# Kernel optimization log

Measured on AMD Instinct MI355X. Metric: run time of the kernel, lower is better.

Reference implementation:

```python
import jax, jax.numpy as jnp
import numpy as np

B, S, D_MODEL, HEADS, DK = 2, 2048, 1024, 16, 64


def setup_inputs() -> dict:
    key = jax.random.key(0)
    ks = jax.random.split(key, 7)
    scale = 0.02
    return {
        "query": jax.random.normal(ks[0], (B, S, D_MODEL), jnp.float32),
        "key": jax.random.normal(ks[1], (B, S, D_MODEL), jnp.float32),
        "value": jax.random.normal(ks[2], (B, S, D_MODEL), jnp.float32),
        "Wq": jax.random.normal(ks[3], (D_MODEL, HEADS * DK), jnp.float32) * scale,
        "bq": jax.random.normal(ks[4], (HEADS * DK,), jnp.float32) * scale,
        "Wo": jax.random.normal(ks[5], (HEADS * DK, D_MODEL), jnp.float32) * scale,
        "bo": jax.random.normal(ks[6], (D_MODEL,), jnp.float32) * scale,
    }


def reference(query, key, value, Wq, bq, Wo, bo):
    # NOTE: faithful to the original code, which (buggily) uses _W_q to
    # project query, key AND value, and scales by sqrt(seq_len), not sqrt(d_k).
    seq_len = key.shape[1]

    def split_heads(x):
        # [B,S,H*DK] -> [H,B,S,DK]; torch chunk(dim=-1)+cat(dim=0) stacks head h
        # (slice h*DK:(h+1)*DK) at batch block h.
        p = x @ Wq + bq
        b, s, _ = p.shape
        return p.reshape(b, s, HEADS, DK).transpose(2, 0, 1, 3)

    q = split_heads(query)   # [H,B,S,DK]
    k = split_heads(key)
    v = split_heads(value)

    inv_scale = jnp.float32(1.0 / np.sqrt(seq_len))
    scores = jnp.einsum("hbqd,hbkd->hbqk", q, k) * inv_scale  # [H,B,S,S]
    attn = jax.nn.softmax(scores, axis=-1)
    out = jnp.einsum("hbqk,hbkd->hbqd", attn, v)  # [H,B,S,DK]
    # inverse of chunk(dim=0)+cat(dim=-1): [H,B,S,DK] -> [B,S,H*DK]
    out = out.transpose(1, 2, 0, 3).reshape(query.shape[0], query.shape[1], HEADS * DK)
    return out @ Wo + bo
```

## Files before the change

### kernel.cpp

```cpp
#include <hip/hip_runtime.h>

#define DEVI __device__ __forceinline__

typedef short short4_t __attribute__((ext_vector_type(4)));
typedef short short8_t __attribute__((ext_vector_type(8)));
typedef __bf16 bf16x8 __attribute__((ext_vector_type(8)));
typedef float f32x4 __attribute__((ext_vector_type(4)));

DEVI short f2bf(float f) {
    union { float f; unsigned u; } v; v.f = f;
    unsigned r = (v.u + 0x7fffu + ((v.u >> 16) & 1u)) >> 16;
    return (short)r;
}

DEVI unsigned pack_ru(float a, float b) {
    union { float f; unsigned u; } x, y; x.f = a; y.f = b;
    return __builtin_amdgcn_perm(y.u + 0x8000u, x.u + 0x8000u, 0x07060302u);
}

DEVI f32x4 pv_mfma(short4_t a, short4_t b, f32x4 c) {
#if defined(__HIP_DEVICE_COMPILE__)
#if __has_builtin(__builtin_amdgcn_mfma_f32_16x16x16bf16_1k)
    return __builtin_amdgcn_mfma_f32_16x16x16bf16_1k(a, b, c, 0, 0, 0);
#else
    union { short8_t s; bf16x8 b; } ua, ub;
    ua.s = (short8_t){a[0], a[1], a[2], a[3], 0, 0, 0, 0};
    ub.s = (short8_t){b[0], b[1], b[2], b[3], 0, 0, 0, 0};
    return __builtin_amdgcn_mfma_f32_16x16x32_bf16(ua.b, ub.b, c, 0, 0, 0);
#endif
#else
    (void)a; (void)b;
    return c;
#endif
}

DEVI void g2lds16(const short* g, short* l) {
    __builtin_amdgcn_global_load_lds(
        (const __attribute__((address_space(1))) void*)g,
        (__attribute__((address_space(3))) void*)l, 16, 0, 0);
}

__global__ __launch_bounds__(256) void cvt3_kernel(const float* __restrict__ q,
                                                   const float* __restrict__ k,
                                                   const float* __restrict__ v,
                                                   short* __restrict__ X) {
    const size_t N1 = (size_t)4096 * 1024;
    size_t e = ((size_t)blockIdx.x * 256 + threadIdx.x) * 4;
    const float* src; size_t off;
    if (e < N1)            { src = q; off = e; }
    else if (e < 2 * N1)   { src = k; off = e - N1; }
    else                   { src = v; off = e - 2 * N1; }
    f32x4 f = *(const f32x4*)(src + off);
    short4_t o;
    o[0] = f2bf(f[0]); o[1] = f2bf(f[1]); o[2] = f2bf(f[2]); o[3] = f2bf(f[3]);
    *(short4_t*)(X + e) = o;
}

__global__ __launch_bounds__(256) void transpose_w_kernel(const float* __restrict__ W,
                                                          short* __restrict__ Wt) {
    __shared__ short T[64][65];
    const int t = threadIdx.x;
    const int kt = blockIdx.x * 64, nt = blockIdx.y * 64;
#pragma unroll
    for (int r = 0; r < 4; ++r) {
        int kl = (t >> 4) + 16 * r;
        int n0 = (t & 15) * 4;
        f32x4 f = *(const f32x4*)(W + (size_t)(kt + kl) * 1024 + nt + n0);
#pragma unroll
        for (int j = 0; j < 4; ++j) T[n0 + j][kl] = f2bf(f[j]);
    }
    __syncthreads();
#pragma unroll
    for (int r = 0; r < 2; ++r) {
        int nl = (t >> 3) + 32 * r;
        int k0 = (t & 7) * 8;
        short8_t v;
#pragma unroll
        for (int j = 0; j < 8; ++j) v[j] = T[nl][k0 + j];
        *(short8_t*)(Wt + (size_t)(nt + nl) * 1024 + kt + k0) = v;
    }
}

template <typename OutT>
__global__ __launch_bounds__(256) void gemm_bt_kernel(const short* __restrict__ A,
                                                      const short* __restrict__ Bt,
                                                      const float* __restrict__ bias,
                                                      OutT* __restrict__ C,
                                                      int M, int N, int K,
                                                      int qrows, float qscale) {
    __shared__ __align__(16) short As[128 * 32];
    __shared__ __align__(16) short Bs[128 * 32];
    const int tid  = threadIdx.x;
    const int lane = tid & 63, wave = tid >> 6;
    const int quad = lane >> 4, l16 = lane & 15;
    const int row0 = blockIdx.x * 128, col0 = blockIdx.y * 128;
    const int wm = (wave >> 1) * 64, wn = (wave & 1) * 64;
    const int srow = lane >> 2;
    const int scol = (lane & 3) * 8;
    f32x4 acc[4][4] = {};
    for (int k0 = 0; k0 < K; k0 += 32) {
#pragma unroll
        for (int r = 0; r < 2; ++r) {
            int rb = r * 64 + wave * 16;
            g2lds16(A  + (size_t)(row0 + rb + srow) * K + k0 + scol, &As[rb * 32]);
            g2lds16(Bt + (size_t)(col0 + rb + srow) * K + k0 + scol, &Bs[rb * 32]);
        }
        __syncthreads();
        bf16x8 af[4], bfr[4];
#pragma unroll
        for (int mi = 0; mi < 4; ++mi) af[mi]  = *(const bf16x8*)&As[(wm + mi * 16 + l16) * 32 + quad * 8];
#pragma unroll
        for (int ni = 0; ni < 4; ++ni) bfr[ni] = *(const bf16x8*)&Bs[(wn + ni * 16 + l16) * 32 + quad * 8];
#pragma unroll
        for (int mi = 0; mi < 4; ++mi)
#pragma unroll
            for (int ni = 0; ni < 4; ++ni)
                acc[mi][ni] = __builtin_amdgcn_mfma_f32_16x16x32_bf16(af[mi], bfr[ni], acc[mi][ni], 0, 0, 0);
        __syncthreads();
    }
#pragma unroll
    for (int mi = 0; mi < 4; ++mi) {
#pragma unroll
        for (int ni = 0; ni < 4; ++ni) {
            int col = col0 + wn + ni * 16 + l16;
            float bv = bias[col];
#pragma unroll
            for (int i = 0; i < 4; ++i) {
                int row = row0 + wm + mi * 16 + quad * 4 + i;
                float val = acc[mi][ni][i] + bv;
                if (row < qrows) val *= qscale;
                if constexpr (sizeof(OutT) == 2) C[(size_t)row * N + col] = (OutT)f2bf(val);
                else                             C[(size_t)row * N + col] = (OutT)val;
            }
        }
    }
}

__global__ __launch_bounds__(256) void transpose_v_kernel(const short* __restrict__ Pv,
                                                          short* __restrict__ VT) {
    __shared__ short T[64][65];
    const int t = threadIdx.x;
    const int hb = blockIdx.x, st = blockIdx.y * 64;
    const int h = hb >> 1, b = hb & 1;
#pragma unroll
    for (int r = 0; r < 2; ++r) {
        int sl = (t >> 3) + 32 * r;
        short8_t v = *(const short8_t*)(Pv + (size_t)(b * 2048 + st + sl) * 1024 + h * 64 + (t & 7) * 8);
#pragma unroll
        for (int j = 0; j < 8; ++j) T[(t & 7) * 8 + j][sl] = v[j];
    }
    __syncthreads();
#pragma unroll
    for (int r = 0; r < 2; ++r) {
        int dl = (t >> 3) + 32 * r;
        short8_t v;
#pragma unroll
        for (int j = 0; j < 8; ++j) v[j] = T[dl][(t & 7) * 8 + j];
        *(short8_t*)(VT + ((size_t)hb * 64 + dl) * 2048 + st + (t & 7) * 8) = v;
    }
}

__global__ __launch_bounds__(256) void attn_kernel(const short* __restrict__ P,
                                                   const short* __restrict__ VT,
                                                   short* __restrict__ O) {
    constexpr int LDK = 72;
    constexpr int LDV = 136;
    constexpr int LDO = 72;
    union SmemU {
        struct { short Ks[2][128 * LDK]; short Vs[2][64 * LDV]; } s;
        short OT[256 * LDO];
    };
    __shared__ __align__(16) SmemU sm;

    const int t = threadIdx.x;
    const int lane = t & 63, wave = t >> 6;
    const int quad = lane >> 4, l16 = lane & 15;
    const int bx = blockIdx.x;
    const int xcd = bx & 7, bi = bx >> 3;
    const int hb = xcd * 4 + (bi & 3), qt = bi >> 2;
    const int h = hb >> 1, b = hb & 1;
    const short* Pq  = P + (size_t)(b * 2048 + qt * 256) * 1024 + h * 64;
    const short* Pk  = P + (size_t)(4096 + b * 2048) * 1024 + h * 64;
    const short* VTh = VT + (size_t)hb * 64 * 2048;
    const int wq = wave * 64;

    bf16x8 qf[4][2];
#pragma unroll
    for (int miq = 0; miq < 4; ++miq)
#pragma unroll
        for (int kh = 0; kh < 2; ++kh)
            qf[miq][kh] = *(const bf16x8*)(Pq + (size_t)(wq + miq * 16 + l16) * 1024 + kh * 32 + quad * 8);

    float lrow[4] = {0.f, 0.f, 0.f, 0.f};
    f32x4 oacc[4][4] = {};

    const int krow = t >> 3, kc8 = (t & 7) * 8;
    const int vrow = t >> 4, vc8 = (t & 15) * 8;

    short8_t kreg[4], vreg[4];
#pragma unroll
    for (int it = 0; it < 4; ++it) {
        kreg[it] = *(const short8_t*)(Pk + (size_t)(it * 32 + krow) * 1024 + kc8);
        vreg[it] = *(const short8_t*)(VTh + (size_t)(it * 16 + vrow) * 2048 + vc8);
    }

    for (int tile = 0; tile < 16; ++tile) {
        const int buf = tile & 1;
        short* Ksb = sm.s.Ks[buf];
        short* Vsb = sm.s.Vs[buf];
#pragma unroll
        for (int it = 0; it < 4; ++it) {
            *(short8_t*)&Ksb[(it * 32 + krow) * LDK + kc8] = kreg[it];
            *(short8_t*)&Vsb[(it * 16 + vrow) * LDV + vc8] = vreg[it];
        }
        __syncthreads();
        if (tile + 1 < 16) {
            int kv0 = (tile + 1) * 128;
#pragma unroll
            for (int it = 0; it < 4; ++it) {
                kreg[it] = *(const short8_t*)(Pk + (size_t)(kv0 + it * 32 + krow) * 1024 + kc8);
                vreg[it] = *(const short8_t*)(VTh + (size_t)(it * 16 + vrow) * 2048 + kv0 + vc8);
            }
        }
#pragma unroll
        for (int kvc = 0; kvc < 8; ++kvc) {
            bf16x8 a0 = *(const bf16x8*)&Ksb[(kvc * 16 + l16) * LDK + quad * 8];
            bf16x8 a1 = *(const bf16x8*)&Ksb[(kvc * 16 + l16) * LDK + 32 + quad * 8];
            short4_t vA[4];
#pragma unroll
            for (int di = 0; di < 4; ++di)
                vA[di] = *(const short4_t*)&Vsb[(di * 16 + l16) * LDV + kvc * 16 + quad * 4];
#pragma unroll
            for (int miq = 0; miq < 4; ++miq) {
                f32x4 s = {};
                s = __builtin_amdgcn_mfma_f32_16x16x32_bf16(a0, qf[miq][0], s, 0, 0, 0);
                s = __builtin_amdgcn_mfma_f32_16x16x32_bf16(a1, qf[miq][1], s, 0, 0, 0);
                float p0 = __builtin_amdgcn_exp2f(s[0]);
                float p1 = __builtin_amdgcn_exp2f(s[1]);
                float p2 = __builtin_amdgcn_exp2f(s[2]);
                float p3 = __builtin_amdgcn_exp2f(s[3]);
                lrow[miq] += (p0 + p1) + (p2 + p3);
                union { uint2 u; short4_t s4; } pb;
                pb.u.x = pack_ru(p0, p1);
                pb.u.y = pack_ru(p2, p3);
#pragma unroll
                for (int di = 0; di < 4; ++di)
                    oacc[di][miq] = pv_mfma(vA[di], pb.s4, oacc[di][miq]);
            }
        }
        __syncthreads();
    }

    float rinv[4];
#pragma unroll
    for (int miq = 0; miq < 4; ++miq) {
        float ls = lrow[miq];
        ls += __shfl_xor(ls, 16);
        ls += __shfl_xor(ls, 32);
        rinv[miq] = 1.0f / ls;
    }
    __syncthreads();

#pragma unroll
    for (int di = 0; di < 4; ++di) {
#pragma unroll
        for (int miq = 0; miq < 4; ++miq) {
            float v0 = oacc[di][miq][0] * rinv[miq];
            float v1 = oacc[di][miq][1] * rinv[miq];
            float v2 = oacc[di][miq][2] * rinv[miq];
            float v3 = oacc[di][miq][3] * rinv[miq];
            uint2 w;
            w.x = pack_ru(v0, v1);
            w.y = pack_ru(v2, v3);
            int q = wq + miq * 16 + l16;
            *(uint2*)&sm.OT[q * LDO + di * 16 + quad * 4] = w;
        }
    }
    __syncthreads();
    {
        short* dst = O + (size_t)(b * 2048 + qt * 256 + t) * 1024 + h * 64;
#pragma unroll
        for (int c = 0; c < 8; ++c)
            *(short8_t*)(dst + c * 8) = *(const short8_t*)&sm.OT[t * LDO + c * 8];
    }
}

extern "C" void kernel_launch(void* const* d_in, const int* in_sizes, int n_in,
                              void* d_out, int out_size, void* d_ws, size_t ws_size,
                              hipStream_t stream) {
    (void)in_sizes; (void)n_in; (void)out_size; (void)ws_size;
    const float* q  = (const float*)d_in[0];
    const float* k  = (const float*)d_in[1];
    const float* v  = (const float*)d_in[2];
    const float* Wq = (const float*)d_in[3];
    const float* bq = (const float*)d_in[4];
    const float* Wo = (const float*)d_in[5];
    const float* bo = (const float*)d_in[6];
    float* out = (float*)d_out;

    short* Xcat = (short*)d_ws;
    short* WqT  = Xcat + (size_t)12288 * 1024;
    short* WoT  = WqT + (size_t)1024 * 1024;
    short* P    = WoT + (size_t)1024 * 1024;
    short* VT   = P + (size_t)12288 * 1024;
    short* O    = VT + (size_t)32 * 64 * 2048;

    const float qscale = 0.022097086912079608f * 1.4426950408889634f;

    cvt3_kernel<<<12288, 256, 0, stream>>>(q, k, v, Xcat);
    transpose_w_kernel<<<dim3(16, 16), 256, 0, stream>>>(Wq, WqT);
    transpose_w_kernel<<<dim3(16, 16), 256, 0, stream>>>(Wo, WoT);
    gemm_bt_kernel<short><<<dim3(96, 8), 256, 0, stream>>>(Xcat, WqT, bq, P, 12288, 1024, 1024, 4096, qscale);
    transpose_v_kernel<<<dim3(32, 32), 256, 0, stream>>>(P + (size_t)8192 * 1024, VT);
    attn_kernel<<<256, 256, 0, stream>>>(P, VT, O);
    gemm_bt_kernel<float><<<dim3(32, 8), 256, 0, stream>>>(O, WoT, bo, out, 4096, 1024, 1024, 0, 1.0f);
}
```

Measured before the change: 227.4 us.

## Split attention KV range in two, add combine pass, smaller-tile output GEMM

The attention kernel now splits each query tile's key/value range into two halves, doubling the grid from 256 to 512 blocks so more CUs are busy. Each half writes unnormalized fp32 partial outputs and row sums, and a new combine kernel adds them, normalizes and converts to bf16. The output projection moves to a new 64x128-tile GEMM to raise its block count. The split adds a full fp32 round trip of the attention output plus an extra launch. It also reuses workspace regions (Xcat, WqT) as scratch, which is safe only because those buffers are dead by then.

```diff
diff --git a/kernel.cpp b/kernel.cpp
--- a/kernel.cpp
+++ b/kernel.cpp
@@ -136,6 +136,59 @@
     }
 }
 
+__global__ __launch_bounds__(256) void gemm_bt64_kernel(const short* __restrict__ A,
+                                                        const short* __restrict__ Bt,
+                                                        const float* __restrict__ bias,
+                                                        float* __restrict__ C,
+                                                        int M, int N, int K) {
+    __shared__ __align__(16) short As[64 * 32];
+    __shared__ __align__(16) short Bs[128 * 32];
+    const int tid  = threadIdx.x;
+    const int lane = tid & 63, wave = tid >> 6;
+    const int quad = lane >> 4, l16 = lane & 15;
+    const int row0 = blockIdx.x * 64, col0 = blockIdx.y * 128;
+    const int wn = wave * 32;
+    const int srow = lane >> 2;
+    const int scol = (lane & 3) * 8;
+    f32x4 acc[4][2] = {};
+    for (int k0 = 0; k0 < K; k0 += 32) {
+        {
+            int rb = wave * 16;
+            g2lds16(A + (size_t)(row0 + rb + srow) * K + k0 + scol, &As[rb * 32]);
+        }
+#pragma unroll
+        for (int r = 0; r < 2; ++r) {
+            int rb = r * 64 + wave * 16;
+            g2lds16(Bt + (size_t)(col0 + rb + srow) * K + k0 + scol, &Bs[rb * 32]);
+        }
+        __syncthreads();
+        bf16x8 af[4], bfr[2];
+#pragma unroll
+        for (int mi = 0; mi < 4; ++mi) af[mi]  = *(const bf16x8*)&As[(mi * 16 + l16) * 32 + quad * 8];
+#pragma unroll
+        for (int ni = 0; ni < 2; ++ni) bfr[ni] = *(const bf16x8*)&Bs[(wn + ni * 16 + l16) * 32 + quad * 8];
+#pragma unroll
+        for (int mi = 0; mi < 4; ++mi)
+#pragma unroll
+            for (int ni = 0; ni < 2; ++ni)
+                acc[mi][ni] = __builtin_amdgcn_mfma_f32_16x16x32_bf16(af[mi], bfr[ni], acc[mi][ni], 0, 0, 0);
+        __syncthreads();
+    }
+#pragma unroll
+    for (int mi = 0; mi < 4; ++mi) {
+#pragma unroll
+        for (int ni = 0; ni < 2; ++ni) {
+            int col = col0 + wn + ni * 16 + l16;
+            float bv = bias[col];
+#pragma unroll
+            for (int i = 0; i < 4; ++i) {
+                int row = row0 + mi * 16 + quad * 4 + i;
+                C[(size_t)row * N + col] = acc[mi][ni][i] + bv;
+            }
+        }
+    }
+}
+
 __global__ __launch_bounds__(256) void transpose_v_kernel(const short* __restrict__ Pv,
                                                           short* __restrict__ VT) {
     __shared__ short T[64][65];
@@ -162,13 +215,15 @@
 
 __global__ __launch_bounds__(256) void attn_kernel(const short* __restrict__ P,
                                                    const short* __restrict__ VT,
-                                                   short* __restrict__ O) {
+                                                   float* __restrict__ Onum0,
+                                                   float* __restrict__ Onum1,
+                                                   float* __restrict__ lpart) {
     constexpr int LDK = 72;
     constexpr int LDV = 136;
-    constexpr int LDO = 72;
+    constexpr int LDOF = 68;
     union SmemU {
         struct { short Ks[2][128 * LDK]; short Vs[2][64 * LDV]; } s;
-        short OT[256 * LDO];
+        float OTf[256 * LDOF];
     };
     __shared__ __align__(16) SmemU sm;
 
@@ -176,12 +231,15 @@
     const int lane = t & 63, wave = t >> 6;
     const int quad = lane >> 4, l16 = lane & 15;
     const int bx = blockIdx.x;
-    const int xcd = bx & 7, bi = bx >> 3;
-    const int hb = xcd * 4 + (bi & 3), qt = bi >> 2;
+    const int xcd = bx & 7, idx = bx >> 3;
+    const int hb = xcd * 4 + (idx & 3);
+    const int rest = idx >> 2;
+    const int qt = rest & 7, split = rest >> 3;
     const int h = hb >> 1, b = hb & 1;
+    const int kvbase = split * 1024;
     const short* Pq  = P + (size_t)(b * 2048 + qt * 256) * 1024 + h * 64;
-    const short* Pk  = P + (size_t)(4096 + b * 2048) * 1024 + h * 64;
-    const short* VTh = VT + (size_t)hb * 64 * 2048;
+    const short* Pk  = P + (size_t)(4096 + b * 2048 + kvbase) * 1024 + h * 64;
+    const short* VTh = VT + (size_t)hb * 64 * 2048 + kvbase;
     const int wq = wave * 64;
 
     bf16x8 qf[4][2];
@@ -204,7 +262,7 @@
         vreg[it] = *(const short8_t*)(VTh + (size_t)(it * 16 + vrow) * 2048 + vc8);
     }
 
-    for (int tile = 0; tile < 16; ++tile) {
+    for (int tile = 0; tile < 8; ++tile) {
         const int buf = tile & 1;
         short* Ksb = sm.s.Ks[buf];
         short* Vsb = sm.s.Vs[buf];
@@ -214,7 +272,7 @@
             *(short8_t*)&Vsb[(it * 16 + vrow) * LDV + vc8] = vreg[it];
         }
         __syncthreads();
-        if (tile + 1 < 16) {
+        if (tile + 1 < 8) {
             int kv0 = (tile + 1) * 128;
 #pragma unroll
             for (int it = 0; it < 4; ++it) {
@@ -251,13 +309,16 @@
         __syncthreads();
     }
 
-    float rinv[4];
+    float* Onum = split ? Onum1 : Onum0;
 #pragma unroll
     for (int miq = 0; miq < 4; ++miq) {
         float ls = lrow[miq];
         ls += __shfl_xor(ls, 16);
         ls += __shfl_xor(ls, 32);
-        rinv[miq] = 1.0f / ls;
+        if (quad == 0) {
+            int row = b * 2048 + qt * 256 + wq + miq * 16 + l16;
+            lpart[(size_t)split * 65536 + row * 16 + h] = ls;
+        }
     }
     __syncthreads();
 
@@ -265,24 +326,34 @@
     for (int di = 0; di < 4; ++di) {
 #pragma unroll
         for (int miq = 0; miq < 4; ++miq) {
-            float v0 = oacc[di][miq][0] * rinv[miq];
-            float v1 = oacc[di][miq][1] * rinv[miq];
-            float v2 = oacc[di][miq][2] * rinv[miq];
-            float v3 = oacc[di][miq][3] * rinv[miq];
-            uint2 w;
-            w.x = pack_ru(v0, v1);
-            w.y = pack_ru(v2, v3);
             int q = wq + miq * 16 + l16;
-            *(uint2*)&sm.OT[q * LDO + di * 16 + quad * 4] = w;
+            *(f32x4*)&sm.OTf[q * LDOF + di * 16 + quad * 4] = oacc[di][miq];
         }
     }
     __syncthreads();
     {
-        short* dst = O + (size_t)(b * 2048 + qt * 256 + t) * 1024 + h * 64;
-#pragma unroll
-        for (int c = 0; c < 8; ++c)
-            *(short8_t*)(dst + c * 8) = *(const short8_t*)&sm.OT[t * LDO + c * 8];
-    }
+        float* dst = Onum + (size_t)(b * 2048 + qt * 256 + t) * 1024 + h * 64;
+#pragma unroll
+        for (int c = 0; c < 16; ++c)
+            *(f32x4*)(dst + c * 4) = *(const f32x4*)&sm.OTf[t * LDOF + c * 4];
+    }
+}
+
+__global__ __launch_bounds__(256) void combine_kernel(const float* __restrict__ n0,
+                                                      const float* __restrict__ n1,
+                                                      const float* __restrict__ lp,
+                                                      short* __restrict__ O) {
+    size_t e = ((size_t)blockIdx.x * 256 + threadIdx.x) * 4;
+    int row = (int)(e >> 10);
+    int hh = ((int)e >> 6) & 15;
+    float l = lp[(size_t)row * 16 + hh] + lp[65536 + (size_t)row * 16 + hh];
+    float r = 1.0f / l;
+    f32x4 a = *(const f32x4*)(n0 + e);
+    f32x4 b = *(const f32x4*)(n1 + e);
+    short4_t o;
+#pragma unroll
+    for (int i = 0; i < 4; ++i) o[i] = f2bf((a[i] + b[i]) * r);
+    *(short4_t*)(O + e) = o;
 }
 
 extern "C" void kernel_launch(void* const* d_in, const int* in_sizes, int n_in,
@@ -304,6 +375,9 @@
     short* P    = WoT + (size_t)1024 * 1024;
     short* VT   = P + (size_t)12288 * 1024;
     short* O    = VT + (size_t)32 * 64 * 2048;
+    float* Onum0 = (float*)Xcat;
+    float* lpart = (float*)WqT;
+    float* Onum1 = (float*)(O + (size_t)4096 * 1024);
 
     const float qscale = 0.022097086912079608f * 1.4426950408889634f;
 
@@ -312,6 +386,7 @@
     transpose_w_kernel<<<dim3(16, 16), 256, 0, stream>>>(Wo, WoT);
     gemm_bt_kernel<short><<<dim3(96, 8), 256, 0, stream>>>(Xcat, WqT, bq, P, 12288, 1024, 1024, 4096, qscale);
     transpose_v_kernel<<<dim3(32, 32), 256, 0, stream>>>(P + (size_t)8192 * 1024, VT);
-    attn_kernel<<<256, 256, 0, stream>>>(P, VT, O);
-    gemm_bt_kernel<float><<<dim3(32, 8), 256, 0, stream>>>(O, WoT, bo, out, 4096, 1024, 1024, 0, 1.0f);
-}
+    attn_kernel<<<512, 256, 0, stream>>>(P, VT, Onum0, Onum1, lpart);
+    combine_kernel<<<4096, 256, 0, stream>>>(Onum0, Onum1, lpart, O);
+    gemm_bt64_kernel<<<dim3(64, 8), 256, 0, stream>>>(O, WoT, bo, out, 4096, 1024, 1024);
+}
```

New measurement: 240.7 us. 5.8% more time.

## Use 8 waves per attention block and smaller-tile output projection GEMM

Applied to the files above, without the earlier changes.

The attention kernel now runs 512 threads per block, so each wave owns 32 query rows instead of 64. That halves per-wave accumulators and registers and doubles the waves resident per CU, meant to improve latency hiding. The output projection moves to a new 64x128-tile GEMM launched on 512 blocks instead of 256, to fill more CUs. The trade-off is more redundant LDS staging per block and a GEMM without double buffering.

```diff
diff --git a/kernel.cpp b/kernel.cpp
--- a/kernel.cpp
+++ b/kernel.cpp
@@ -136,6 +136,59 @@
     }
 }
 
+__global__ __launch_bounds__(256) void gemm_bt64_kernel(const short* __restrict__ A,
+                                                        const short* __restrict__ Bt,
+                                                        const float* __restrict__ bias,
+                                                        float* __restrict__ C,
+                                                        int M, int N, int K) {
+    __shared__ __align__(16) short As[64 * 32];
+    __shared__ __align__(16) short Bs[128 * 32];
+    const int tid  = threadIdx.x;
+    const int lane = tid & 63, wave = tid >> 6;
+    const int quad = lane >> 4, l16 = lane & 15;
+    const int row0 = blockIdx.x * 64, col0 = blockIdx.y * 128;
+    const int wn = wave * 32;
+    const int srow = lane >> 2;
+    const int scol = (lane & 3) * 8;
+    f32x4 acc[4][2] = {};
+    for (int k0 = 0; k0 < K; k0 += 32) {
+        {
+            int rb = wave * 16;
+            g2lds16(A + (size_t)(row0 + rb + srow) * K + k0 + scol, &As[rb * 32]);
+        }
+#pragma unroll
+        for (int r = 0; r < 2; ++r) {
+            int rb = r * 64 + wave * 16;
+            g2lds16(Bt + (size_t)(col0 + rb + srow) * K + k0 + scol, &Bs[rb * 32]);
+        }
+        __syncthreads();
+        bf16x8 af[4], bfr[2];
+#pragma unroll
+        for (int mi = 0; mi < 4; ++mi) af[mi]  = *(const bf16x8*)&As[(mi * 16 + l16) * 32 + quad * 8];
+#pragma unroll
+        for (int ni = 0; ni < 2; ++ni) bfr[ni] = *(const bf16x8*)&Bs[(wn + ni * 16 + l16) * 32 + quad * 8];
+#pragma unroll
+        for (int mi = 0; mi < 4; ++mi)
+#pragma unroll
+            for (int ni = 0; ni < 2; ++ni)
+                acc[mi][ni] = __builtin_amdgcn_mfma_f32_16x16x32_bf16(af[mi], bfr[ni], acc[mi][ni], 0, 0, 0);
+        __syncthreads();
+    }
+#pragma unroll
+    for (int mi = 0; mi < 4; ++mi) {
+#pragma unroll
+        for (int ni = 0; ni < 2; ++ni) {
+            int col = col0 + wn + ni * 16 + l16;
+            float bv = bias[col];
+#pragma unroll
+            for (int i = 0; i < 4; ++i) {
+                int row = row0 + mi * 16 + quad * 4 + i;
+                C[(size_t)row * N + col] = acc[mi][ni][i] + bv;
+            }
+        }
+    }
+}
+
 __global__ __launch_bounds__(256) void transpose_v_kernel(const short* __restrict__ Pv,
                                                           short* __restrict__ VT) {
     __shared__ short T[64][65];
@@ -160,9 +213,9 @@
     }
 }
 
-__global__ __launch_bounds__(256) void attn_kernel(const short* __restrict__ P,
-                                                   const short* __restrict__ VT,
-                                                   short* __restrict__ O) {
+__global__ __launch_bounds__(512, 2) void attn_kernel(const short* __restrict__ P,
+                                                      const short* __restrict__ VT,
+                                                      short* __restrict__ O) {
     constexpr int LDK = 72;
     constexpr int LDV = 136;
     constexpr int LDO = 72;
@@ -182,26 +235,26 @@
     const short* Pq  = P + (size_t)(b * 2048 + qt * 256) * 1024 + h * 64;
     const short* Pk  = P + (size_t)(4096 + b * 2048) * 1024 + h * 64;
     const short* VTh = VT + (size_t)hb * 64 * 2048;
-    const int wq = wave * 64;
-
-    bf16x8 qf[4][2];
-#pragma unroll
-    for (int miq = 0; miq < 4; ++miq)
+    const int wq = wave * 32;
+
+    bf16x8 qf[2][2];
+#pragma unroll
+    for (int miq = 0; miq < 2; ++miq)
 #pragma unroll
         for (int kh = 0; kh < 2; ++kh)
             qf[miq][kh] = *(const bf16x8*)(Pq + (size_t)(wq + miq * 16 + l16) * 1024 + kh * 32 + quad * 8);
 
-    float lrow[4] = {0.f, 0.f, 0.f, 0.f};
-    f32x4 oacc[4][4] = {};
+    float lrow[2] = {0.f, 0.f};
+    f32x4 oacc[4][2] = {};
 
     const int krow = t >> 3, kc8 = (t & 7) * 8;
     const int vrow = t >> 4, vc8 = (t & 15) * 8;
 
-    short8_t kreg[4], vreg[4];
-#pragma unroll
-    for (int it = 0; it < 4; ++it) {
-        kreg[it] = *(const short8_t*)(Pk + (size_t)(it * 32 + krow) * 1024 + kc8);
-        vreg[it] = *(const short8_t*)(VTh + (size_t)(it * 16 + vrow) * 2048 + vc8);
+    short8_t kreg[2], vreg[2];
+#pragma unroll
+    for (int it = 0; it < 2; ++it) {
+        kreg[it] = *(const short8_t*)(Pk + (size_t)(it * 64 + krow) * 1024 + kc8);
+        vreg[it] = *(const short8_t*)(VTh + (size_t)(it * 32 + vrow) * 2048 + vc8);
     }
 
     for (int tile = 0; tile < 16; ++tile) {
@@ -209,17 +262,17 @@
         short* Ksb = sm.s.Ks[buf];
         short* Vsb = sm.s.Vs[buf];
 #pragma unroll
-        for (int it = 0; it < 4; ++it) {
-            *(short8_t*)&Ksb[(it * 32 + krow) * LDK + kc8] = kreg[it];
-            *(short8_t*)&Vsb[(it * 16 + vrow) * LDV + vc8] = vreg[it];
+        for (int it = 0; it < 2; ++it) {
+            *(short8_t*)&Ksb[(it * 64 + krow) * LDK + kc8] = kreg[it];
+            *(short8_t*)&Vsb[(it * 32 + vrow) * LDV + vc8] = vreg[it];
         }
         __syncthreads();
         if (tile + 1 < 16) {
             int kv0 = (tile + 1) * 128;
 #pragma unroll
-            for (int it = 0; it < 4; ++it) {
-                kreg[it] = *(const short8_t*)(Pk + (size_t)(kv0 + it * 32 + krow) * 1024 + kc8);
-                vreg[it] = *(const short8_t*)(VTh + (size_t)(it * 16 + vrow) * 2048 + kv0 + vc8);
+            for (int it = 0; it < 2; ++it) {
+                kreg[it] = *(const short8_t*)(Pk + (size_t)(kv0 + it * 64 + krow) * 1024 + kc8);
+                vreg[it] = *(const short8_t*)(VTh + (size_t)(it * 32 + vrow) * 2048 + kv0 + vc8);
             }
         }
 #pragma unroll
@@ -231,7 +284,7 @@
             for (int di = 0; di < 4; ++di)
                 vA[di] = *(const short4_t*)&Vsb[(di * 16 + l16) * LDV + kvc * 16 + quad * 4];
 #pragma unroll
-            for (int miq = 0; miq < 4; ++miq) {
+            for (int miq = 0; miq < 2; ++miq) {
                 f32x4 s = {};
                 s = __builtin_amdgcn_mfma_f32_16x16x32_bf16(a0, qf[miq][0], s, 0, 0, 0);
                 s = __builtin_amdgcn_mfma_f32_16x16x32_bf16(a1, qf[miq][1], s, 0, 0, 0);
@@ -251,20 +304,19 @@
         __syncthreads();
     }
 
-    float rinv[4];
-#pragma unroll
-    for (int miq = 0; miq < 4; ++miq) {
+    float rinv[2];
+#pragma unroll
+    for (int miq = 0; miq < 2; ++miq) {
         float ls = lrow[miq];
         ls += __shfl_xor(ls, 16);
         ls += __shfl_xor(ls, 32);
         rinv[miq] = 1.0f / ls;
     }
-    __syncthreads();
 
 #pragma unroll
     for (int di = 0; di < 4; ++di) {
 #pragma unroll
-        for (int miq = 0; miq < 4; ++miq) {
+        for (int miq = 0; miq < 2; ++miq) {
             float v0 = oacc[di][miq][0] * rinv[miq];
             float v1 = oacc[di][miq][1] * rinv[miq];
             float v2 = oacc[di][miq][2] * rinv[miq];
@@ -278,10 +330,11 @@
     }
     __syncthreads();
     {
-        short* dst = O + (size_t)(b * 2048 + qt * 256 + t) * 1024 + h * 64;
-#pragma unroll
-        for (int c = 0; c < 8; ++c)
-            *(short8_t*)(dst + c * 8) = *(const short8_t*)&sm.OT[t * LDO + c * 8];
+        const int orow = t >> 1, ocol = (t & 1) * 32;
+        short* dst = O + (size_t)(b * 2048 + qt * 256 + orow) * 1024 + h * 64 + ocol;
+#pragma unroll
+        for (int c = 0; c < 4; ++c)
+            *(short8_t*)(dst + c * 8) = *(const short8_t*)&sm.OT[orow * LDO + ocol + c * 8];
     }
 }
 
@@ -312,6 +365,6 @@
     transpose_w_kernel<<<dim3(16, 16), 256, 0, stream>>>(Wo, WoT);
     gemm_bt_kernel<short><<<dim3(96, 8), 256, 0, stream>>>(Xcat, WqT, bq, P, 12288, 1024, 1024, 4096, qscale);
     transpose_v_kernel<<<dim3(32, 32), 256, 0, stream>>>(P + (size_t)8192 * 1024, VT);
-    attn_kernel<<<256, 256, 0, stream>>>(P, VT, O);
-    gemm_bt_kernel<float><<<dim3(32, 8), 256, 0, stream>>>(O, WoT, bo, out, 4096, 1024, 1024, 0, 1.0f);
-}
+    attn_kernel<<<256, 512, 0, stream>>>(P, VT, O);
+    gemm_bt64_kernel<<<dim3(64, 8), 256, 0, stream>>>(O, WoT, bo, out, 4096, 1024, 1024);
+}
```

After: 219.8 us. 1.03x faster.
